# Optimization experiments

Hardware: AMD Instinct MI355X
Metric: run time of the kernel (lower is better)

## Reference

```python
import jax, jax.numpy as jnp
import numpy as np

N, M = 4096, 256

def setup_inputs() -> dict:
    key = jax.random.key(0)
    k1, k2 = jax.random.split(key)
    y_pred = jax.random.normal(k1, (N, M), dtype=jnp.float32)
    y = jax.random.normal(k2, (N, 1), dtype=jnp.float32)
    return {"y_pred": y_pred, "y": y}

def reference(y_pred, y):
    n, m = y_pred.shape
    # MAE term: mean(|y_pred - y|), y broadcast over ensemble dim
    mae_loss = jnp.mean(jnp.abs(y_pred - y))
    # Ensemble spread term: sum_{i,k,l} |x[i,k] - x[i,l]| / (n * 2 * m^2)
    # pairwise diffs: [n, m, m]
    pair = jnp.abs(y_pred[:, None, :] - y_pred[:, :, None])
    mix_loss = jnp.sum(pair) / (n * 2 * m ** 2)
    return mae_loss - mix_loss
```

## Files before the change

### kernel.cpp

```cpp
#include <hip/hip_runtime.h>


constexpr int N_ROWS = 4096;
constexpr int M_COLS = 256;
constexpr int ROWS_PER_BLOCK = 4;
constexpr int NUM_BLOCKS = N_ROWS / ROWS_PER_BLOCK;

__device__ __forceinline__ void abs_acc(float& m, float a, float b) {
    float t = a - b;
    asm("v_add_f32 %0, %0, |%1|" : "+v"(m) : "v"(t));
}

__global__ __launch_bounds__(256)
void crps_partial(const float* __restrict__ y_pred,
                  const float* __restrict__ y,
                  float* __restrict__ partial) {
    __shared__ __align__(16) float4 rows[ROWS_PER_BLOCK][2 * M_COLS / 4];
    __shared__ float wsum[ROWS_PER_BLOCK];

    const int wave = threadIdx.x >> 6;
    const int lane = threadIdx.x & 63;
    const int row  = blockIdx.x * ROWS_PER_BLOCK + wave;

    const float4 xk = reinterpret_cast<const float4*>(y_pred + row * M_COLS)[lane];
    rows[wave][lane]      = xk;
    rows[wave][lane + 64] = xk;
    const float yi = y[row];

    const float xo[4] = {xk.x, xk.y, xk.z, xk.w};

    float mae = 0.0f;
    #pragma unroll
    for (int j = 0; j < 4; ++j) abs_acc(mae, xo[j], yi);

    float m[4] = {0.0f, 0.0f, 0.0f, 0.0f};
    abs_acc(m[0], xo[0], xo[1]); abs_acc(m[1], xo[0], xo[2]);
    abs_acc(m[2], xo[0], xo[3]); abs_acc(m[3], xo[1], xo[2]);
    abs_acc(m[0], xo[1], xo[3]); abs_acc(m[1], xo[2], xo[3]);

    const float4* r4 = &rows[wave][lane];

    #pragma unroll 8
    for (int s = 1; s <= 24; ++s) {
        const float4 v = r4[s];
        #pragma unroll
        for (int j = 0; j < 4; ++j) {
            abs_acc(m[j], xo[j], v.x); abs_acc(m[j], xo[j], v.y);
            abs_acc(m[j], xo[j], v.z); abs_acc(m[j], xo[j], v.w);
        }
    }
    #pragma unroll
    for (int s = 25; s <= 31; ++s) {
        const float4 v = r4[s];
        #pragma unroll
        for (int j = 0; j < 4; ++j) {
            abs_acc(m[j], xo[j], v.x); abs_acc(m[j], xo[j], v.y);
            abs_acc(m[j], xo[j], v.z); abs_acc(m[j], xo[j], v.w);
        }
    }
    float m32 = 0.0f;
    {
        const float4 v = r4[32];
        #pragma unroll
        for (int j = 0; j < 4; ++j) {
            abs_acc(m32, xo[j], v.x); abs_acc(m32, xo[j], v.y);
            abs_acc(m32, xo[j], v.z); abs_acc(m32, xo[j], v.w);
        }
    }

    const float msum = (m[0] + m[1]) + (m[2] + m[3]);

    constexpr float mae_scale = 1.0f / ((float)N_ROWS * (float)M_COLS);
    constexpr float inv_NM2   = 1.0f / ((float)N_ROWS * (float)M_COLS * (float)M_COLS);
    float part = mae * mae_scale - (msum + 0.5f * m32) * inv_NM2;

    #pragma unroll
    for (int off = 32; off > 0; off >>= 1)
        part += __shfl_down(part, off, 64);

    if (lane == 0) wsum[wave] = part;
    __syncthreads();
    if (threadIdx.x == 0)
        partial[blockIdx.x] = (wsum[0] + wsum[1]) + (wsum[2] + wsum[3]);
}

__global__ __launch_bounds__(256)
void crps_final(const float* __restrict__ partial, float* __restrict__ out) {
    __shared__ float wsum[4];
    const int t = threadIdx.x;
    const float4 v4 = reinterpret_cast<const float4*>(partial)[t];
    float v = (v4.x + v4.y) + (v4.z + v4.w);
    #pragma unroll
    for (int off = 32; off > 0; off >>= 1)
        v += __shfl_down(v, off, 64);
    if ((t & 63) == 0) wsum[t >> 6] = v;
    __syncthreads();
    if (t == 0)
        *out = (wsum[0] + wsum[1]) + (wsum[2] + wsum[3]);
}

extern "C" void kernel_launch(void* const* d_in, const int* in_sizes, int n_in,
                              void* d_out, int out_size, void* d_ws, size_t ws_size,
                              hipStream_t stream) {
    const float* y_pred = (const float*)d_in[0];
    const float* y      = (const float*)d_in[1];
    float* out          = (float*)d_out;
    float* ws           = (float*)d_ws;

    crps_partial<<<NUM_BLOCKS, 256, 0, stream>>>(y_pred, y, ws);
    crps_final<<<1, 256, 0, stream>>>(ws, out);
}
```

Measured before the change: 62.00 us.

## Replace pairwise abs-diff sum with in-register bitonic sort and rank-weighted sum

Replaces the O(m^2) pairwise absolute-difference accumulation, which staged each row in shared memory, with a per-row bitonic sort done in registers through wave shuffles. The mix term is then computed as a rank-weighted sum of the sorted values, sum over ranks of (2r - m + 1) times x_(r). This cuts the arithmetic from 256 pairwise ops per element to O(log^2 m) compare-exchange and shuffle steps. It trades simple ALU work for many cross-lane shuffles and changes the floating-point summation order.

```diff
diff --git a/kernel.cpp b/kernel.cpp
--- a/kernel.cpp
+++ b/kernel.cpp
@@ -15,7 +15,6 @@
 void crps_partial(const float* __restrict__ y_pred,
                   const float* __restrict__ y,
                   float* __restrict__ partial) {
-    __shared__ __align__(16) float4 rows[ROWS_PER_BLOCK][2 * M_COLS / 4];
     __shared__ float wsum[ROWS_PER_BLOCK];
 
     const int wave = threadIdx.x >> 6;
@@ -23,56 +22,65 @@
     const int row  = blockIdx.x * ROWS_PER_BLOCK + wave;
 
     const float4 xk = reinterpret_cast<const float4*>(y_pred + row * M_COLS)[lane];
-    rows[wave][lane]      = xk;
-    rows[wave][lane + 64] = xk;
     const float yi = y[row];
 
-    const float xo[4] = {xk.x, xk.y, xk.z, xk.w};
+    float v[4] = {xk.x, xk.y, xk.z, xk.w};
 
     float mae = 0.0f;
     #pragma unroll
-    for (int j = 0; j < 4; ++j) abs_acc(mae, xo[j], yi);
+    for (int j = 0; j < 4; ++j) abs_acc(mae, v[j], yi);
 
-    float m[4] = {0.0f, 0.0f, 0.0f, 0.0f};
-    abs_acc(m[0], xo[0], xo[1]); abs_acc(m[1], xo[0], xo[2]);
-    abs_acc(m[2], xo[0], xo[3]); abs_acc(m[3], xo[1], xo[2]);
-    abs_acc(m[0], xo[1], xo[3]); abs_acc(m[1], xo[2], xo[3]);
+    auto CE = [&](int a, int b) {
+        const float mn = fminf(v[a], v[b]);
+        const float mx = fmaxf(v[a], v[b]);
+        v[a] = mn; v[b] = mx;
+    };
 
-    const float4* r4 = &rows[wave][lane];
+    CE(0,1); CE(2,3);
+    CE(0,3); CE(1,2);
+    CE(0,1); CE(2,3);
 
-    #pragma unroll 8
-    for (int s = 1; s <= 24; ++s) {
-        const float4 v = r4[s];
+    #pragma unroll
+    for (int k = 8; k <= 256; k <<= 1) {
+        {
+            const int  lm  = (k >> 2) - 1;
+            const bool isl = (lane & (k >> 3)) == 0;
+            const float p0 = __shfl_xor(v[3], lm, 64);
+            const float p1 = __shfl_xor(v[2], lm, 64);
+            const float p2 = __shfl_xor(v[1], lm, 64);
+            const float p3 = __shfl_xor(v[0], lm, 64);
+            v[0] = isl ? fminf(v[0], p0) : fmaxf(v[0], p0);
+            v[1] = isl ? fminf(v[1], p1) : fmaxf(v[1], p1);
+            v[2] = isl ? fminf(v[2], p2) : fmaxf(v[2], p2);
+            v[3] = isl ? fminf(v[3], p3) : fmaxf(v[3], p3);
+        }
         #pragma unroll
-        for (int j = 0; j < 4; ++j) {
-            abs_acc(m[j], xo[j], v.x); abs_acc(m[j], xo[j], v.y);
-            abs_acc(m[j], xo[j], v.z); abs_acc(m[j], xo[j], v.w);
+        for (int j = k >> 2; j >= 4; j >>= 1) {
+            const int  lm  = j >> 2;
+            const bool isl = (lane & lm) == 0;
+            const float p0 = __shfl_xor(v[0], lm, 64);
+            const float p1 = __shfl_xor(v[1], lm, 64);
+            const float p2 = __shfl_xor(v[2], lm, 64);
+            const float p3 = __shfl_xor(v[3], lm, 64);
+            v[0] = isl ? fminf(v[0], p0) : fmaxf(v[0], p0);
+            v[1] = isl ? fminf(v[1], p1) : fmaxf(v[1], p1);
+            v[2] = isl ? fminf(v[2], p2) : fmaxf(v[2], p2);
+            v[3] = isl ? fminf(v[3], p3) : fmaxf(v[3], p3);
         }
-    }
-    #pragma unroll
-    for (int s = 25; s <= 31; ++s) {
-        const float4 v = r4[s];
-        #pragma unroll
-        for (int j = 0; j < 4; ++j) {
-            abs_acc(m[j], xo[j], v.x); abs_acc(m[j], xo[j], v.y);
-            abs_acc(m[j], xo[j], v.z); abs_acc(m[j], xo[j], v.w);
-        }
-    }
-    float m32 = 0.0f;
-    {
-        const float4 v = r4[32];
-        #pragma unroll
-        for (int j = 0; j < 4; ++j) {
-            abs_acc(m32, xo[j], v.x); abs_acc(m32, xo[j], v.y);
-            abs_acc(m32, xo[j], v.z); abs_acc(m32, xo[j], v.w);
-        }
+        CE(0,2); CE(1,3);
+        CE(0,1); CE(2,3);
     }
 
-    const float msum = (m[0] + m[1]) + (m[2] + m[3]);
+    const float wbase = (float)(8 * lane - 255);
+    float mix;
+    mix = v[0] * wbase;
+    mix = fmaf(v[1], wbase + 2.0f, mix);
+    mix = fmaf(v[2], wbase + 4.0f, mix);
+    mix = fmaf(v[3], wbase + 6.0f, mix);
 
     constexpr float mae_scale = 1.0f / ((float)N_ROWS * (float)M_COLS);
     constexpr float inv_NM2   = 1.0f / ((float)N_ROWS * (float)M_COLS * (float)M_COLS);
-    float part = mae * mae_scale - (msum + 0.5f * m32) * inv_NM2;
+    float part = mae * mae_scale - mix * inv_NM2;
 
     #pragma unroll
     for (int off = 32; off > 0; off >>= 1)
```

After: 62.81 us. No clear change (+1.3%).
